# Kernel optimization log

Measured on AMD Instinct MI355X. Metric: run time of the kernel, lower is better.

The kernel has to match this reference:

```python
import jax, jax.numpy as jnp
from jax import lax
import numpy as np

B = 8192   # samples
L = 32     # predicted chars per sample (num_chars[i])
M = 32     # target labels per sample (num_labels[i])
C = 96     # character classes


def _edit_trace(pred, tgt):
    """Levenshtein DP + backtrace for one sample.
    pred: [L] int, tgt: [M] int.
    Returns (ti, tj, valid) of length L+M: 1-based (i,j) positions of the
    diagonal (match/substitute) moves on the optimal edit path, as emitted by
    distance_and_trace; valid masks non-diagonal / out-of-path steps."""
    Ls, Ms = pred.shape[0], tgt.shape[0]
    cost = (pred[:, None] != tgt[None, :]).astype(jnp.int32)  # [L,M]
    row0 = jnp.arange(Ms + 1, dtype=jnp.int32)

    def row_step(prev, crow):
        first = prev[0] + 1
        def col_step(left, z):
            up, diag, c = z
            v = jnp.minimum(jnp.minimum(up + 1, left + 1), diag + c)
            return v, v
        _, rest = lax.scan(col_step, first, (prev[1:], prev[:-1], crow))
        new = jnp.concatenate([first[None], rest])
        return new, new

    _, rows = lax.scan(row_step, row0, cost)
    D = jnp.concatenate([row0[None, :], rows], axis=0)  # [L+1, M+1]

    def bt_step(carry, _):
        i, j = carry
        c = cost[jnp.maximum(i - 1, 0), jnp.maximum(j - 1, 0)]
        dij = D[i, j]
        diag = (i > 0) & (j > 0) & (D[i - 1, j - 1] + c == dij)
        up = (~diag) & (i > 0) & (D[i - 1, j] + 1 == dij)
        left = (~diag) & (~up) & (j > 0)
        ni = i - (diag | up).astype(jnp.int32)
        nj = j - (diag | left).astype(jnp.int32)
        return (ni, nj), (i, j, diag)

    (_, _), (ti, tj, valid) = lax.scan(
        bt_step, (jnp.int32(Ls), jnp.int32(Ms)), None, length=Ls + Ms)
    return ti, tj, valid


def _forward(x, y, num_chars, num_labels):
    b = num_chars.shape[0]
    c = x.shape[1]
    l = x.shape[0] // b
    m = y.shape[0] // b
    logits = x.reshape(b, l, c)          # [B,L,C]
    labels = y.reshape(b, m)             # [B,M]
    pred = jnp.argmax(logits, axis=-1)   # torch.max(x,1) indices
    ti, tj, valid = jax.vmap(_edit_trace)(pred, labels)  # [B, L+M] each
    logp = jax.nn.log_softmax(logits, axis=-1)
    xi = jnp.where(valid, ti - 1, 0)     # trace[:,0]-1 (+ per-sample offset via reshape)
    yi = jnp.where(valid, tj - 1, 0)     # trace[:,1]-1
    lab = jnp.take_along_axis(labels, yi, axis=1)                 # [B,L+M]
    lp = jnp.take_along_axis(logp, xi[..., None], axis=1)         # [B,L+M,C]
    ce = -jnp.take_along_axis(lp, lab[..., None], axis=2)[..., 0]  # [B,L+M]
    cnt = valid.sum(axis=1)
    per_sample = jnp.where(valid, ce, 0.0).sum(axis=1) / jnp.maximum(cnt, 1)
    nonempty = cnt > 0                   # attenuation: skip empty traces
    total = jnp.where(nonempty, per_sample, 0.0).sum()
    return total / nonempty.sum()


def setup_inputs() -> dict:
    key = jax.random.key(0)
    k1, k2 = jax.random.split(key)
    x = jax.random.normal(k1, (B * L, C), dtype=jnp.float32)
    y = jax.random.randint(k2, (B * M,), 0, C, dtype=jnp.int32)
    num_chars = jnp.full((B,), L, dtype=jnp.int32)
    num_labels = jnp.full((B,), M, dtype=jnp.int32)
    return {"x": x, "y": y, "num_chars": num_chars, "num_labels": num_labels}


def reference(x, y, num_chars, num_labels):
    return _forward(x, y, num_chars, num_labels)
```

## Files before the change

### kernel.cpp

```cpp
#include <hip/hip_runtime.h>
#include <hip/hip_bf16.h>
#include <stdint.h>

#define BNUM  8192
#define LROWS 32
#define MLAB  32
#define CCLS  96
#define WPB   4
#define SPW   2
#define SPB   (WPB*SPW)
#define NBLK  (BNUM/SPB)

__global__ __launch_bounds__(256) void editloss_main(
    const float* __restrict__ x, const int* __restrict__ y,
    float* __restrict__ partial_sum, float* __restrict__ partial_cnt)
{
    __shared__ float ceTab[SPB][LROWS * MLAB];
    __shared__ float psum[SPB];
    __shared__ float pcnt[SPB];

    const int w    = threadIdx.x >> 6;
    const int lane = threadIdx.x & 63;
    const int g    = lane >> 5;
    const int u    = lane & 31;
    const int s    = w * SPW + g;
    const int sb   = blockIdx.x * SPB + s;

    const float* xs    = x + (size_t)sb * (LROWS * CCLS);
    const int    lab_u = y[sb * MLAB + u];

    for (int r = 0; r < LROWS; ++r) {
        const float* row = xs + r * CCLS;
        const float v0 = row[u * 3 + 0];
        const float v1 = row[u * 3 + 1];
        const float v2 = row[u * 3 + 2];
        const float xg = row[lab_u];
        float m = fmaxf(fmaxf(v0, v1), v2);
#pragma unroll
        for (int t = 16; t >= 1; t >>= 1) m = fmaxf(m, __shfl_xor(m, t));
        int cand = (v0 == m) ? (u * 3)
                 : (v1 == m) ? (u * 3 + 1)
                 : (v2 == m) ? (u * 3 + 2) : 4096;
#pragma unroll
        for (int t = 16; t >= 1; t >>= 1) cand = min(cand, __shfl_xor(cand, t));
        float se = __expf(v0 - m) + __expf(v1 - m) + __expf(v2 - m);
#pragma unroll
        for (int t = 16; t >= 1; t >>= 1) se += __shfl_xor(se, t);
        const float lse = m + __logf(se);
        const float ce  = lse - xg;
        ceTab[s][r * MLAB + u] = (cand == lab_u) ? ce : -ce;
    }
    __syncthreads();

    const int j = u + 1;
    int   prevW = 0;   float prevCE = 0.f;
    int   diagW = 0;   float diagCE = 0.f;
    for (int d = 1; d <= LROWS + MLAB; ++d) {
        const int   lWs  = __shfl_up(prevW, 1);
        const float lCEs = __shfl_up(prevCE, 1);
        const int i = d - j;
        const int   lW  = (u == 0) ? max(i, 0)     : lWs;
        const float lCE = (u == 0) ? 0.f           : lCEs;
        const int   dW  = (u == 0) ? max(i - 1, 0) : diagW;
        const float dCE = (u == 0) ? 0.f           : diagCE;
        int curW; float curCE;
        if (i <= 0) {
            curW = j; curCE = 0.f;
        } else if (i > LROWS) {
            curW = prevW; curCE = prevCE;
        } else {
            const int uD = prevW & 255, uC = prevW >> 8;
            const int lD = lW & 255,    lC = lW >> 8;
            const int dD = dW & 255,    dC = dW >> 8;
            const float ct  = ceTab[s][(i - 1) * MLAB + (j - 1)];
            const int   c   = (ct < 0.f) ? 1 : 0;
            const float cev = fabsf(ct);
            const int nD = min(min(uD, lD) + 1, dD + c);
            const bool dg = (dD + c == nD);
            const bool up = !dg && (uD + 1 == nD);
            int nC; float nCE;
            if (dg)      { nC = dC + 1; nCE = dCE + cev; }
            else if (up) { nC = uC;     nCE = prevCE;    }
            else         { nC = lC;     nCE = lCE;       }
            curW = nD | (nC << 8);
            curCE = nCE;
        }
        diagW = lWs; diagCE = lCEs;
        prevW = curW; prevCE = curCE;
    }

    if (u == 31) {
        const int cnt = prevW >> 8;
        psum[s] = (cnt > 0) ? prevCE / (float)cnt : 0.f;
        pcnt[s] = (cnt > 0) ? 1.f : 0.f;
    }
    __syncthreads();
    if (threadIdx.x == 0) {
        float ss = 0.f, cc = 0.f;
#pragma unroll
        for (int k = 0; k < SPB; ++k) { ss += psum[k]; cc += pcnt[k]; }
        partial_sum[blockIdx.x] = ss;
        partial_cnt[blockIdx.x] = cc;
    }
}

__global__ __launch_bounds__(256) void editloss_finalize(
    const float* __restrict__ partial_sum, const float* __restrict__ partial_cnt,
    float* __restrict__ out, int nblocks)
{
    float s = 0.f, c = 0.f;
    for (int k = threadIdx.x; k < nblocks; k += 256) {
        s += partial_sum[k];
        c += partial_cnt[k];
    }
#pragma unroll
    for (int d = 32; d >= 1; d >>= 1) {
        s += __shfl_xor(s, d);
        c += __shfl_xor(c, d);
    }
    __shared__ float ss[4], cc[4];
    const int w = threadIdx.x >> 6, lane = threadIdx.x & 63;
    if (lane == 0) { ss[w] = s; cc[w] = c; }
    __syncthreads();
    if (threadIdx.x == 0) {
        const float S  = ss[0] + ss[1] + ss[2] + ss[3];
        const float C2 = cc[0] + cc[1] + cc[2] + cc[3];
        out[0] = (C2 > 0.f) ? (S / C2) : 0.f;
    }
}

extern "C" void kernel_launch(void* const* d_in, const int* in_sizes, int n_in,
                              void* d_out, int out_size, void* d_ws, size_t ws_size,
                              hipStream_t stream) {
    const float* x = (const float*)d_in[0];
    const int*   y = (const int*)d_in[1];
    float* out = (float*)d_out;

    float* partial_sum = (float*)d_ws;
    float* partial_cnt = partial_sum + NBLK;

    editloss_main<<<NBLK, 256, 0, stream>>>(x, y, partial_sum, partial_cnt);
    editloss_finalize<<<1, 256, 0, stream>>>(partial_sum, partial_cnt, out, NBLK);
}
```

Measured before the change: 176.3 us.

## Compute per-row argmax and logsumexp in one lane with float4 loads

Softmax statistics are reorganised so that each lane owns one logits row instead of spreading every row across 32 lanes. Each lane reads its row with float4 loads and computes argmax and the exp-sum in registers, which removes three 5-step shuffle reductions for each of the 32 rows. The row results go through shared memory to the lanes that build the cost/CE table, and the label logit is gathered separately. Block barriers are replaced by LDS waitcnt fences, and launch bounds and an unroll pragma are added to the DP loop. In exchange, the row-per-lane loads are strided rather than coalesced, and logsumexp no longer subtracts the row max, so large logits could overflow.

```diff
diff --git a/kernel.cpp b/kernel.cpp
--- a/kernel.cpp
+++ b/kernel.cpp
@@ -1,5 +1,4 @@
 #include <hip/hip_runtime.h>
-#include <hip/hip_bf16.h>
 #include <stdint.h>
 
 #define BNUM  8192
@@ -11,13 +10,14 @@
 #define SPB   (WPB*SPW)
 #define NBLK  (BNUM/SPB)
 
-__global__ __launch_bounds__(256) void editloss_main(
+__global__ __launch_bounds__(256, 4) void editloss_main(
     const float* __restrict__ x, const int* __restrict__ y,
     float* __restrict__ partial_sum, float* __restrict__ partial_cnt)
 {
-    __shared__ float ceTab[SPB][LROWS * MLAB];
-    __shared__ float psum[SPB];
-    __shared__ float pcnt[SPB];
+    __shared__ float  ceTab[SPB][LROWS * MLAB];
+    __shared__ float2 lpS[SPB][LROWS];
+    __shared__ float  psum[SPB];
+    __shared__ float  pcnt[SPB];
 
     const int w    = threadIdx.x >> 6;
     const int lane = threadIdx.x & 63;
@@ -29,32 +29,49 @@
     const float* xs    = x + (size_t)sb * (LROWS * CCLS);
     const int    lab_u = y[sb * MLAB + u];
 
-    for (int r = 0; r < LROWS; ++r) {
-        const float* row = xs + r * CCLS;
-        const float v0 = row[u * 3 + 0];
-        const float v1 = row[u * 3 + 1];
-        const float v2 = row[u * 3 + 2];
-        const float xg = row[lab_u];
-        float m = fmaxf(fmaxf(v0, v1), v2);
+    {
+        const float4* rowv = (const float4*)(xs + (size_t)u * CCLS);
+        float bmax[4]; int bidx[4]; float bsum[4];
 #pragma unroll
-        for (int t = 16; t >= 1; t >>= 1) m = fmaxf(m, __shfl_xor(m, t));
-        int cand = (v0 == m) ? (u * 3)
-                 : (v1 == m) ? (u * 3 + 1)
-                 : (v2 == m) ? (u * 3 + 2) : 4096;
+        for (int c = 0; c < 4; ++c) { bmax[c] = -1e30f; bidx[c] = 0; bsum[c] = 0.f; }
 #pragma unroll
-        for (int t = 16; t >= 1; t >>= 1) cand = min(cand, __shfl_xor(cand, t));
-        float se = __expf(v0 - m) + __expf(v1 - m) + __expf(v2 - m);
+        for (int c = 0; c < 4; ++c) {
 #pragma unroll
-        for (int t = 16; t >= 1; t >>= 1) se += __shfl_xor(se, t);
-        const float lse = m + __logf(se);
-        const float ce  = lse - xg;
-        ceTab[s][r * MLAB + u] = (cand == lab_u) ? ce : -ce;
+            for (int k = 0; k < 6; ++k) {
+                const float4 v = rowv[c * 6 + k];
+                const int base = (c * 6 + k) * 4;
+                if (v.x > bmax[c]) { bmax[c] = v.x; bidx[c] = base + 0; }
+                if (v.y > bmax[c]) { bmax[c] = v.y; bidx[c] = base + 1; }
+                if (v.z > bmax[c]) { bmax[c] = v.z; bidx[c] = base + 2; }
+                if (v.w > bmax[c]) { bmax[c] = v.w; bidx[c] = base + 3; }
+                bsum[c] += __expf(v.x) + __expf(v.y) + __expf(v.z) + __expf(v.w);
+            }
+        }
+        float m = bmax[0]; int idx = bidx[0];
+#pragma unroll
+        for (int c = 1; c < 4; ++c)
+            if (bmax[c] > m) { m = bmax[c]; idx = bidx[c]; }
+        const float lse = __logf((bsum[0] + bsum[1]) + (bsum[2] + bsum[3]));
+        lpS[s][u] = make_float2(lse, (float)idx);
     }
-    __syncthreads();
+    asm volatile("s_waitcnt lgkmcnt(0)" ::: "memory");
+
+    {
+        const float* gcol = xs + lab_u;
+#pragma unroll
+        for (int r = 0; r < LROWS; ++r) {
+            const float2 lp = lpS[s][r];
+            const float  xg = gcol[r * CCLS];
+            const float  ce = lp.x - xg;
+            ceTab[s][r * MLAB + u] = ((int)lp.y == lab_u) ? ce : -ce;
+        }
+    }
+    asm volatile("s_waitcnt lgkmcnt(0)" ::: "memory");
 
     const int j = u + 1;
     int   prevW = 0;   float prevCE = 0.f;
     int   diagW = 0;   float diagCE = 0.f;
+#pragma unroll 4
     for (int d = 1; d <= LROWS + MLAB; ++d) {
         const int   lWs  = __shfl_up(prevW, 1);
         const float lCEs = __shfl_up(prevCE, 1);
@@ -72,16 +89,15 @@
             const int uD = prevW & 255, uC = prevW >> 8;
             const int lD = lW & 255,    lC = lW >> 8;
             const int dD = dW & 255,    dC = dW >> 8;
-            const float ct  = ceTab[s][(i - 1) * MLAB + (j - 1)];
+            const float ct  = ceTab[s][(i - 1) * MLAB + u];
             const int   c   = (ct < 0.f) ? 1 : 0;
-            const float cev = fabsf(ct);
             const int nD = min(min(uD, lD) + 1, dD + c);
             const bool dg = (dD + c == nD);
             const bool up = !dg && (uD + 1 == nD);
             int nC; float nCE;
-            if (dg)      { nC = dC + 1; nCE = dCE + cev; }
-            else if (up) { nC = uC;     nCE = prevCE;    }
-            else         { nC = lC;     nCE = lCE;       }
+            if (dg)      { nC = dC + 1; nCE = dCE + fabsf(ct); }
+            else if (up) { nC = uC;     nCE = prevCE;          }
+            else         { nC = lC;     nCE = lCE;             }
             curW = nD | (nC << 8);
             curCE = nCE;
         }
```

Measured after the change: 169.0 us. 1.04x faster.
